# Kernel tuning notes

Hardware: AMD Instinct MI355X
Metric: run time of the kernel (lower is better)

## Reference

```python
import jax, jax.numpy as jnp
from jax import lax
import numpy as np

INPUT_SIZE = 1
HIDDEN = 96


def _lstm_layer(x_seq, W_ih, W_hh, b_ih, b_hh):
    # x_seq: [T, B, I]; W_ih: [4H, I]; W_hh: [4H, H]; gate order i,f,g,o (torch)
    T, B, _ = x_seq.shape
    H = W_hh.shape[1]
    # precompute input contribution for all timesteps (the only big GEMM)
    xg = jnp.einsum('tbi,gi->tbg', x_seq, W_ih) + b_ih + b_hh  # [T, B, 4H]

    def step(carry, xg_t):
        h, c = carry
        g = xg_t + h @ W_hh.T  # [B, 4H]
        i, f, gg, o = jnp.split(g, 4, axis=-1)
        i = jax.nn.sigmoid(i)
        f = jax.nn.sigmoid(f)
        gg = jnp.tanh(gg)
        o = jax.nn.sigmoid(o)
        c = f * c + i * gg
        h = o * jnp.tanh(c)
        return (h, c), h

    init = (jnp.zeros((B, H), x_seq.dtype), jnp.zeros((B, H), x_seq.dtype))
    _, hs = lax.scan(step, init, xg)
    return hs  # [T, B, H]


def setup_inputs() -> dict:
    key = jax.random.key(0)
    ks = jax.random.split(key, 11)
    B, T = 256, 1024
    H, I = HIDDEN, INPUT_SIZE
    s_in = 1.0 / np.sqrt(H)  # torch LSTM init scale
    u = lambda k, shape: jax.random.uniform(k, shape, jnp.float32, -s_in, s_in)
    return {
        'x': jax.random.normal(ks[0], (B, T, I), jnp.float32),
        'W_ih0': u(ks[1], (4 * H, I)),
        'W_hh0': u(ks[2], (4 * H, H)),
        'b_ih0': u(ks[3], (4 * H,)),
        'b_hh0': u(ks[4], (4 * H,)),
        'W_ih1': u(ks[5], (4 * H, H)),
        'W_hh1': u(ks[6], (4 * H, H)),
        'b_ih1': u(ks[7], (4 * H,)),
        'b_hh1': u(ks[8], (4 * H,)),
        'Wl': u(ks[9], (1, H)),
        'bl': u(ks[10], (1,)),
    }


def reference(x, W_ih0, W_hh0, b_ih0, b_hh0, W_ih1, W_hh1, b_ih1, b_hh1, Wl, bl):
    xt = jnp.transpose(x, (1, 0, 2))  # [T, B, I]
    h1 = _lstm_layer(xt, W_ih0, W_hh0, b_ih0, b_hh0)  # [T, B, H]
    h2 = _lstm_layer(h1, W_ih1, W_hh1, b_ih1, b_hh1)  # [T, B, H]
    out = jnp.einsum('tbh,oh->tbo', h2, Wl) + bl  # [T, B, 1]
    return jnp.transpose(out, (1, 0, 2))  # [B, T, 1]
```

## Files before the change

kernel.cpp:

```cpp
#include <hip/hip_runtime.h>

#define TLEN   1024
#define HID    96
#define NSAMP  16
#define NTHR   512
#define CHUNK  16
#define NCHUNK (TLEN / CHUNK)
#define DEPTH  8
#define HSTR   104
#define HBUF   (NSAMP * HSTR)
#define SLOTH  (CHUNK * NSAMP * HSTR)
#define XSTR   1025
#define OSTR   1025

typedef _Float16 f16x8 __attribute__((ext_vector_type(8)));
typedef float    f32x4 __attribute__((ext_vector_type(4)));

__device__ __forceinline__ float sigf(float v) {
    float e = __builtin_amdgcn_exp2f(v * -1.44269504089f);
    return __builtin_amdgcn_rcpf(1.0f + e);
}
__device__ __forceinline__ float tanh_fast(float v) {
    float e = __builtin_amdgcn_exp2f(v * 2.88539008178f);
    return fmaf(-2.0f, __builtin_amdgcn_rcpf(e + 1.0f), 1.0f);
}

__device__ __forceinline__ f16x8 cvt_frag(const float* base) {
    const float4* q = reinterpret_cast<const float4*>(base);
    float4 v0 = q[0], v1 = q[1];
    f16x8 r;
    r[0] = (_Float16)v0.x; r[1] = (_Float16)v0.y;
    r[2] = (_Float16)v0.z; r[3] = (_Float16)v0.w;
    r[4] = (_Float16)v1.x; r[5] = (_Float16)v1.y;
    r[6] = (_Float16)v1.z; r[7] = (_Float16)v1.w;
    return r;
}

extern "C" __global__ void zero_flags(int* p) { p[threadIdx.x] = 0; }

extern "C" __global__ void __launch_bounds__(NTHR)
lstm2_split(const float* __restrict__ x,
            const float* __restrict__ Wih0, const float* __restrict__ Whh0,
            const float* __restrict__ bih0, const float* __restrict__ bhh0,
            const float* __restrict__ Wih1, const float* __restrict__ Whh1,
            const float* __restrict__ bih1, const float* __restrict__ bhh1,
            const float* __restrict__ Wl,   const float* __restrict__ bl,
            float* __restrict__ out, unsigned char* __restrict__ ws)
{
    __shared__ __attribute__((aligned(16))) unsigned char lds_raw[127040];
    float*    xo_s  = (float*)lds_raw;
    _Float16* cbuf  = (_Float16*)(lds_raw + 65600);
    _Float16* dbuf  = (_Float16*)(lds_raw + 65600 + 53248);
    float4*   btab  = (float4*)(lds_raw + 65600 + 53248 + 6656);

    int*      prog     = (int*)ws;
    int*      consumed = (int*)(ws + 2048);
    _Float16* ring     = (_Float16*)(ws + 4096);

    const int tid  = threadIdx.x;
    const int lane = tid & 63;
    const int wv   = tid >> 6;
    const int n    = lane & 15;
    const int kg   = lane >> 4;
    const int blk  = blockIdx.x;
    const bool isS1 = (blk < 16);
    const int g    = isS1 ? blk : blk - 16;
    _Float16* gring = ring + (size_t)g * DEPTH * SLOTH;

    if (isS1) {
        for (int i = tid; i < NSAMP * TLEN; i += NTHR) {
            int s = i >> 10, t = i & (TLEN - 1);
            xo_s[s * XSTR + t] = x[(g * NSAMP + s) * TLEN + t];
        }
        if (tid < HID)
            btab[tid] = make_float4(bih0[tid]       + bhh0[tid],
                                    bih0[ 96 + tid] + bhh0[ 96 + tid],
                                    bih0[192 + tid] + bhh0[192 + tid],
                                    bih0[288 + tid] + bhh0[288 + tid]);
    } else {
        for (int i = tid; i < NSAMP * OSTR; i += NTHR) xo_s[i] = 0.0f;
        if (tid < HID)
            btab[tid] = make_float4(bih1[tid]       + bhh1[tid],
                                    bih1[ 96 + tid] + bhh1[ 96 + tid],
                                    bih1[192 + tid] + bhh1[192 + tid],
                                    bih1[288 + tid] + bhh1[288 + tid]);
    }
    for (int i = tid; i < 2 * HBUF; i += NTHR) dbuf[i] = (_Float16)0.0f;

    f16x8 A[3][6];
    float aux[3][4];
    #pragma unroll
    for (int mi = 0; mi < 3; ++mi) {
        const int tile = wv * 3 + mi;
        const int rp   = tile * 16 + n;
        const int orow = (rp & 3) * HID + (rp >> 2);
        const int u    = tile * 4 + kg;
        if (isS1) {
            A[mi][0] = cvt_frag(Whh0 + orow * HID +  0 + kg * 8);
            A[mi][1] = cvt_frag(Whh0 + orow * HID + 32 + kg * 8);
            A[mi][2] = cvt_frag(Whh0 + orow * HID + 64 + kg * 8);
            A[mi][3] = A[mi][0]; A[mi][4] = A[mi][1]; A[mi][5] = A[mi][2];
            aux[mi][0] = Wih0[u];           aux[mi][1] = Wih0[ 96 + u];
            aux[mi][2] = Wih0[192 + u];     aux[mi][3] = Wih0[288 + u];
        } else {
            A[mi][0] = cvt_frag(Wih1 + orow * HID +  0 + kg * 8);
            A[mi][1] = cvt_frag(Wih1 + orow * HID + 32 + kg * 8);
            A[mi][2] = cvt_frag(Wih1 + orow * HID + 64 + kg * 8);
            A[mi][3] = cvt_frag(Whh1 + orow * HID +  0 + kg * 8);
            A[mi][4] = cvt_frag(Whh1 + orow * HID + 32 + kg * 8);
            A[mi][5] = cvt_frag(Whh1 + orow * HID + 64 + kg * 8);
            aux[mi][0] = Wl[u]; aux[mi][1] = 0.f; aux[mi][2] = 0.f; aux[mi][3] = 0.f;
        }
    }
    float cst[3] = {0.f, 0.f, 0.f};
    __syncthreads();

    if (isS1) {
        for (int ch = 0; ch < NCHUNK; ++ch) {
            #pragma unroll 1
            for (int s = 0; s < CHUNK; ++s) {
                const int t = ch * CHUNK + s;
                const int rd = t & 1, wb = rd ^ 1;
                const _Float16* hr = dbuf + rd * HBUF + n * HSTR + kg * 8;
                f16x8 B0 = *reinterpret_cast<const f16x8*>(hr);
                f16x8 B1 = *reinterpret_cast<const f16x8*>(hr + 32);
                f16x8 B2 = *reinterpret_cast<const f16x8*>(hr + 64);
                const float xt = xo_s[n * XSTR + t];
                _Float16* hw = dbuf + wb * HBUF + n * HSTR;
                _Float16* cw = cbuf + (s * NSAMP + n) * HSTR;
                #pragma unroll
                for (int mi = 0; mi < 3; ++mi) {
                    f32x4 acc = {0.f, 0.f, 0.f, 0.f};
                    acc = __builtin_amdgcn_mfma_f32_16x16x32_f16(A[mi][0], B0, acc, 0, 0, 0);
                    acc = __builtin_amdgcn_mfma_f32_16x16x32_f16(A[mi][1], B1, acc, 0, 0, 0);
                    acc = __builtin_amdgcn_mfma_f32_16x16x32_f16(A[mi][2], B2, acc, 0, 0, 0);
                    const int up = (wv * 3 + mi) * 4 + kg;
                    float4 bb = btab[up];
                    float gi = sigf(fmaf(aux[mi][0], xt, acc[0] + bb.x));
                    float gf = sigf(fmaf(aux[mi][1], xt, acc[1] + bb.y));
                    float gg = tanh_fast(fmaf(aux[mi][2], xt, acc[2] + bb.z));
                    float go = sigf(fmaf(aux[mi][3], xt, acc[3] + bb.w));
                    cst[mi] = gf * cst[mi] + gi * gg;
                    _Float16 h1v = (_Float16)(go * tanh_fast(cst[mi]));
                    hw[up] = h1v;
                    cw[up] = h1v;
                }
                __syncthreads();
            }
            if (tid == 0) {
                while (ch - __hip_atomic_load(&consumed[g * 16], __ATOMIC_ACQUIRE,
                                              __HIP_MEMORY_SCOPE_AGENT) >= DEPTH)
                    __builtin_amdgcn_s_sleep(2);
            }
            __syncthreads();
            {
                _Float16* slot = gring + (size_t)(ch % DEPTH) * SLOTH;
                const int4* src = (const int4*)cbuf;
                int4* dst = (int4*)slot;
                for (int i = tid; i < (int)(SLOTH * 2 / 16); i += NTHR) dst[i] = src[i];
            }
            __threadfence();
            __syncthreads();
            if (tid == 0)
                __hip_atomic_store(&prog[g * 16], ch + 1, __ATOMIC_RELEASE,
                                   __HIP_MEMORY_SCOPE_AGENT);
        }
    } else {
        for (int ch = 0; ch < NCHUNK; ++ch) {
            if (tid == 0) {
                while (__hip_atomic_load(&prog[g * 16], __ATOMIC_ACQUIRE,
                                         __HIP_MEMORY_SCOPE_AGENT) < ch + 1)
                    __builtin_amdgcn_s_sleep(2);
            }
            __syncthreads();
            {
                const _Float16* slot = gring + (size_t)(ch % DEPTH) * SLOTH;
                const int4* src = (const int4*)slot;
                int4* dst = (int4*)cbuf;
                for (int i = tid; i < (int)(SLOTH * 2 / 16); i += NTHR) dst[i] = src[i];
            }
            __syncthreads();
            if (tid == 0)
                __hip_atomic_store(&consumed[g * 16], ch + 1, __ATOMIC_RELEASE,
                                   __HIP_MEMORY_SCOPE_AGENT);
            #pragma unroll 1
            for (int s = 0; s < CHUNK; ++s) {
                const int t = ch * CHUNK + s;
                const int rd = t & 1, wb = rd ^ 1;
                const _Float16* p1 = cbuf + (s * NSAMP + n) * HSTR + kg * 8;
                const _Float16* p2 = dbuf + rd * HBUF + n * HSTR + kg * 8;
                f16x8 B0 = *reinterpret_cast<const f16x8*>(p1);
                f16x8 B1 = *reinterpret_cast<const f16x8*>(p1 + 32);
                f16x8 B2 = *reinterpret_cast<const f16x8*>(p1 + 64);
                f16x8 B3 = *reinterpret_cast<const f16x8*>(p2);
                f16x8 B4 = *reinterpret_cast<const f16x8*>(p2 + 32);
                f16x8 B5 = *reinterpret_cast<const f16x8*>(p2 + 64);
                _Float16* hw = dbuf + wb * HBUF + n * HSTR;
                float po = 0.f;
                #pragma unroll
                for (int mi = 0; mi < 3; ++mi) {
                    f32x4 acc = {0.f, 0.f, 0.f, 0.f};
                    acc = __builtin_amdgcn_mfma_f32_16x16x32_f16(A[mi][0], B0, acc, 0, 0, 0);
                    acc = __builtin_amdgcn_mfma_f32_16x16x32_f16(A[mi][1], B1, acc, 0, 0, 0);
                    acc = __builtin_amdgcn_mfma_f32_16x16x32_f16(A[mi][2], B2, acc, 0, 0, 0);
                    acc = __builtin_amdgcn_mfma_f32_16x16x32_f16(A[mi][3], B3, acc, 0, 0, 0);
                    acc = __builtin_amdgcn_mfma_f32_16x16x32_f16(A[mi][4], B4, acc, 0, 0, 0);
                    acc = __builtin_amdgcn_mfma_f32_16x16x32_f16(A[mi][5], B5, acc, 0, 0, 0);
                    const int up = (wv * 3 + mi) * 4 + kg;
                    float4 bb = btab[up];
                    float gi = sigf(acc[0] + bb.x);
                    float gf = sigf(acc[1] + bb.y);
                    float gg = tanh_fast(acc[2] + bb.z);
                    float go = sigf(acc[3] + bb.w);
                    cst[mi] = gf * cst[mi] + gi * gg;
                    float h2v = go * tanh_fast(cst[mi]);
                    hw[up] = (_Float16)h2v;
                    po = fmaf(aux[mi][0], h2v, po);
                }
                po += __shfl_xor(po, 16);
                po += __shfl_xor(po, 32);
                if (lane < 16) atomicAdd(&xo_s[n * OSTR + t], po);
                __syncthreads();
            }
        }
        const float bl0 = bl[0];
        for (int i = tid; i < NSAMP * TLEN; i += NTHR) {
            int s = i >> 10, t = i & (TLEN - 1);
            out[(g * NSAMP + s) * TLEN + t] = xo_s[s * OSTR + t] + bl0;
        }
    }
}

extern "C" void kernel_launch(void* const* d_in, const int* in_sizes, int n_in,
                              void* d_out, int out_size, void* d_ws, size_t ws_size,
                              hipStream_t stream)
{
    (void)in_sizes; (void)n_in; (void)ws_size; (void)out_size;
    const float* x    = (const float*)d_in[0];
    const float* Wih0 = (const float*)d_in[1];
    const float* Whh0 = (const float*)d_in[2];
    const float* bih0 = (const float*)d_in[3];
    const float* bhh0 = (const float*)d_in[4];
    const float* Wih1 = (const float*)d_in[5];
    const float* Whh1 = (const float*)d_in[6];
    const float* bih1 = (const float*)d_in[7];
    const float* bhh1 = (const float*)d_in[8];
    const float* Wl   = (const float*)d_in[9];
    const float* bl   = (const float*)d_in[10];

    zero_flags<<<dim3(1), dim3(1024), 0, stream>>>((int*)d_ws);
    lstm2_split<<<dim3(32), dim3(NTHR), 0, stream>>>(
        x, Wih0, Whh0, bih0, bhh0, Wih1, Whh1, bih1, bhh1, Wl, bl,
        (float*)d_out, (unsigned char*)d_ws);
}
```

Before: 1.094 ms.

## Overlap ring-buffer copies with recurrent steps in both LSTM stages

Stage 1 now waits for a free ring slot before computing a chunk and copies each timestep's h1 slice to global memory during the following step, instead of copying the whole chunk after it finishes. Stage 2 double-buffers the chunk in LDS and, when the producer already has the next chunk ready, prefetches it slice by slice while computing the current one. Stage 2 also writes outputs per chunk from a small LDS buffer instead of keeping a full-sequence output array, which frees LDS for the second chunk buffer. The aim is to hide global-memory transfer and handoff latency behind the serial recurrence, at the cost of more complex flag logic and extra per-step work inside the latency-critical loop.

Result: faster. 1.063 ms (-2.9%).

```diff
diff --git a/kernel.cpp b/kernel.cpp
--- a/kernel.cpp
+++ b/kernel.cpp
@@ -9,9 +9,10 @@
 #define DEPTH  8
 #define HSTR   104
 #define HBUF   (NSAMP * HSTR)
-#define SLOTH  (CHUNK * NSAMP * HSTR)
+#define SLICE  (NSAMP * HSTR)
+#define SLICE4 208
+#define SLOTH  (CHUNK * SLICE)
 #define XSTR   1025
-#define OSTR   1025
 
 typedef _Float16 f16x8 __attribute__((ext_vector_type(8)));
 typedef float    f32x4 __attribute__((ext_vector_type(4)));
@@ -47,11 +48,7 @@
             const float* __restrict__ Wl,   const float* __restrict__ bl,
             float* __restrict__ out, unsigned char* __restrict__ ws)
 {
-    __shared__ __attribute__((aligned(16))) unsigned char lds_raw[127040];
-    float*    xo_s  = (float*)lds_raw;
-    _Float16* cbuf  = (_Float16*)(lds_raw + 65600);
-    _Float16* dbuf  = (_Float16*)(lds_raw + 65600 + 53248);
-    float4*   btab  = (float4*)(lds_raw + 65600 + 53248 + 6656);
+    __shared__ __attribute__((aligned(16))) unsigned char lds_raw[127104];
 
     int*      prog     = (int*)ws;
     int*      consumed = (int*)(ws + 2048);
@@ -67,10 +64,19 @@
     const int g    = isS1 ? blk : blk - 16;
     _Float16* gring = ring + (size_t)g * DEPTH * SLOTH;
 
+    float*    x_s  = (float*)lds_raw;
+    _Float16* cbS1 = (_Float16*)(lds_raw + 65600);
+    _Float16* cb0  = (_Float16*)lds_raw;
+    _Float16* cb1  = (_Float16*)(lds_raw + 53248);
+    _Float16* dbuf = (_Float16*)(lds_raw + (isS1 ? 118848 : 106496));
+    float4*   btab = (float4*)(lds_raw + (isS1 ? 125504 : 113152));
+    float*    obuf = (float*)(lds_raw + 114688);
+    int*      nf_s = (int*)(lds_raw + 115776);
+
     if (isS1) {
         for (int i = tid; i < NSAMP * TLEN; i += NTHR) {
             int s = i >> 10, t = i & (TLEN - 1);
-            xo_s[s * XSTR + t] = x[(g * NSAMP + s) * TLEN + t];
+            x_s[s * XSTR + t] = x[(g * NSAMP + s) * TLEN + t];
         }
         if (tid < HID)
             btab[tid] = make_float4(bih0[tid]       + bhh0[tid],
@@ -78,7 +84,6 @@
                                     bih0[192 + tid] + bhh0[192 + tid],
                                     bih0[288 + tid] + bhh0[288 + tid]);
     } else {
-        for (int i = tid; i < NSAMP * OSTR; i += NTHR) xo_s[i] = 0.0f;
         if (tid < HID)
             btab[tid] = make_float4(bih1[tid]       + bhh1[tid],
                                     bih1[ 96 + tid] + bhh1[ 96 + tid],
@@ -117,17 +122,29 @@
 
     if (isS1) {
         for (int ch = 0; ch < NCHUNK; ++ch) {
+            if (tid == 0) {
+                while (ch - __hip_atomic_load(&consumed[g * 16], __ATOMIC_ACQUIRE,
+                                              __HIP_MEMORY_SCOPE_AGENT) >= DEPTH)
+                    __builtin_amdgcn_s_sleep(2);
+            }
+            __syncthreads();
+            _Float16* slot = gring + (size_t)(ch % DEPTH) * SLOTH;
             #pragma unroll 1
             for (int s = 0; s < CHUNK; ++s) {
+                if (s > 0 && tid < SLICE4) {
+                    const int4* src = (const int4*)(cbS1 + (s - 1) * SLICE);
+                    int4* dst = (int4*)(slot + (s - 1) * SLICE);
+                    dst[tid] = src[tid];
+                }
                 const int t = ch * CHUNK + s;
                 const int rd = t & 1, wb = rd ^ 1;
                 const _Float16* hr = dbuf + rd * HBUF + n * HSTR + kg * 8;
                 f16x8 B0 = *reinterpret_cast<const f16x8*>(hr);
                 f16x8 B1 = *reinterpret_cast<const f16x8*>(hr + 32);
                 f16x8 B2 = *reinterpret_cast<const f16x8*>(hr + 64);
-                const float xt = xo_s[n * XSTR + t];
+                const float xt = x_s[n * XSTR + t];
                 _Float16* hw = dbuf + wb * HBUF + n * HSTR;
-                _Float16* cw = cbuf + (s * NSAMP + n) * HSTR;
+                _Float16* cw = cbS1 + s * SLICE + n * HSTR;
                 #pragma unroll
                 for (int mi = 0; mi < 3; ++mi) {
                     f32x4 acc = {0.f, 0.f, 0.f, 0.f};
@@ -147,17 +164,10 @@
                 }
                 __syncthreads();
             }
-            if (tid == 0) {
-                while (ch - __hip_atomic_load(&consumed[g * 16], __ATOMIC_ACQUIRE,
-                                              __HIP_MEMORY_SCOPE_AGENT) >= DEPTH)
-                    __builtin_amdgcn_s_sleep(2);
-            }
-            __syncthreads();
-            {
-                _Float16* slot = gring + (size_t)(ch % DEPTH) * SLOTH;
-                const int4* src = (const int4*)cbuf;
-                int4* dst = (int4*)slot;
-                for (int i = tid; i < (int)(SLOTH * 2 / 16); i += NTHR) dst[i] = src[i];
+            if (tid < SLICE4) {
+                const int4* src = (const int4*)(cbS1 + 15 * SLICE);
+                int4* dst = (int4*)(slot + 15 * SLICE);
+                dst[tid] = src[tid];
             }
             __threadfence();
             __syncthreads();
@@ -166,28 +176,49 @@
                                    __HIP_MEMORY_SCOPE_AGENT);
         }
     } else {
+        const float bl0 = bl[0];
+        int cur = 0;
+        bool have = false;
         for (int ch = 0; ch < NCHUNK; ++ch) {
-            if (tid == 0) {
-                while (__hip_atomic_load(&prog[g * 16], __ATOMIC_ACQUIRE,
-                                         __HIP_MEMORY_SCOPE_AGENT) < ch + 1)
-                    __builtin_amdgcn_s_sleep(2);
-            }
-            __syncthreads();
-            {
+            _Float16* ccur = cur ? cb1 : cb0;
+            _Float16* cnxt = cur ? cb0 : cb1;
+            if (!have) {
+                if (tid == 0) {
+                    while (__hip_atomic_load(&prog[g * 16], __ATOMIC_ACQUIRE,
+                                             __HIP_MEMORY_SCOPE_AGENT) < ch + 1)
+                        __builtin_amdgcn_s_sleep(2);
+                }
+                __syncthreads();
                 const _Float16* slot = gring + (size_t)(ch % DEPTH) * SLOTH;
                 const int4* src = (const int4*)slot;
-                int4* dst = (int4*)cbuf;
-                for (int i = tid; i < (int)(SLOTH * 2 / 16); i += NTHR) dst[i] = src[i];
-            }
-            __syncthreads();
-            if (tid == 0)
-                __hip_atomic_store(&consumed[g * 16], ch + 1, __ATOMIC_RELEASE,
-                                   __HIP_MEMORY_SCOPE_AGENT);
+                int4* dst = (int4*)ccur;
+                for (int i = tid; i < CHUNK * SLICE4; i += NTHR) dst[i] = src[i];
+                __syncthreads();
+                if (tid == 0)
+                    __hip_atomic_store(&consumed[g * 16], ch + 1, __ATOMIC_RELEASE,
+                                       __HIP_MEMORY_SCOPE_AGENT);
+            }
+            if (tid < CHUNK * 17) obuf[tid] = 0.0f;
+            if (tid == 0) {
+                int r = 0;
+                if (ch + 1 < NCHUNK)
+                    r = (__hip_atomic_load(&prog[g * 16], __ATOMIC_ACQUIRE,
+                                           __HIP_MEMORY_SCOPE_AGENT) >= ch + 2) ? 1 : 0;
+                *nf_s = r;
+            }
+            __syncthreads();
+            const bool pf = (*nf_s != 0);
+            const _Float16* nslot = gring + (size_t)((ch + 1) % DEPTH) * SLOTH;
             #pragma unroll 1
             for (int s = 0; s < CHUNK; ++s) {
+                if (pf && tid < SLICE4) {
+                    const int4* src = (const int4*)(nslot + s * SLICE);
+                    int4* dst = (int4*)(cnxt + s * SLICE);
+                    dst[tid] = src[tid];
+                }
                 const int t = ch * CHUNK + s;
                 const int rd = t & 1, wb = rd ^ 1;
-                const _Float16* p1 = cbuf + (s * NSAMP + n) * HSTR + kg * 8;
+                const _Float16* p1 = ccur + s * SLICE + n * HSTR + kg * 8;
                 const _Float16* p2 = dbuf + rd * HBUF + n * HSTR + kg * 8;
                 f16x8 B0 = *reinterpret_cast<const f16x8*>(p1);
                 f16x8 B1 = *reinterpret_cast<const f16x8*>(p1 + 32);
@@ -219,14 +250,23 @@
                 }
                 po += __shfl_xor(po, 16);
                 po += __shfl_xor(po, 32);
-                if (lane < 16) atomicAdd(&xo_s[n * OSTR + t], po);
-                __syncthreads();
-            }
-        }
-        const float bl0 = bl[0];
-        for (int i = tid; i < NSAMP * TLEN; i += NTHR) {
-            int s = i >> 10, t = i & (TLEN - 1);
-            out[(g * NSAMP + s) * TLEN + t] = xo_s[s * OSTR + t] + bl0;
+                if (lane < 16) atomicAdd(&obuf[s * 17 + n], po);
+                __syncthreads();
+            }
+            if (tid < 256) {
+                int s = tid & 15, j = tid >> 4;
+                out[(g * NSAMP + j) * TLEN + ch * CHUNK + s] = obuf[s * 17 + j] + bl0;
+            }
+            if (pf) {
+                if (tid == 0)
+                    __hip_atomic_store(&consumed[g * 16], ch + 2, __ATOMIC_RELEASE,
+                                       __HIP_MEMORY_SCOPE_AGENT);
+                cur ^= 1;
+                have = true;
+            } else {
+                have = false;
+            }
+            __syncthreads();
         }
     }
 }
```
